# Optimization experiments

Measured on AMD Instinct MI355X. Metric: run time of the kernel, lower is better.

## Reference

```python
import jax, jax.numpy as jnp
import numpy as np

HEADS = 4
DIM_HEAD = 32  # total inner dim; per-head dim = DIM_HEAD // HEADS = 8
SCALE = DIM_HEAD ** -0.5  # faithful to original: scale uses dim_head, not per-head dim


def setup_inputs() -> dict:
    key = jax.random.key(0)
    k_x, k_q, k_kv, k_o, k_pe = jax.random.split(key, 5)
    B, L, dim = 131072, 4, 256
    inner = DIM_HEAD
    x = jax.random.normal(k_x, (B, L, dim), dtype=jnp.float32)
    Wq = jax.random.normal(k_q, (dim, inner), dtype=jnp.float32) * 0.02
    Wkv = jax.random.normal(k_kv, (dim, 2 * inner), dtype=jnp.float32) * 0.02
    Wo = jax.random.normal(k_o, (inner, dim), dtype=jnp.float32) * 0.02
    bo = jnp.zeros((dim,), dtype=jnp.float32)
    pos_emb = jax.random.normal(k_pe, (1, HEADS, L, L), dtype=jnp.float32)
    return {"x": x, "Wq": Wq, "Wkv": Wkv, "Wo": Wo, "bo": bo, "pos_emb": pos_emb}


def reference(x, Wq, Wkv, Wo, bo, pos_emb):
    B, L, dim = x.shape
    dh = DIM_HEAD // HEADS  # per-head dim
    q = x @ Wq                       # [B, L, inner]
    kv = x @ Wkv                     # [B, L, 2*inner]
    k, v = jnp.split(kv, 2, axis=-1)
    # [B, L, inner] -> [B, heads, L, dh]
    split_heads = lambda t: t.reshape(B, L, HEADS, dh).transpose(0, 2, 1, 3)
    q, k, v = map(split_heads, (q, k, v))
    q = q * SCALE
    sim = jnp.einsum('bhid,bhjd->bhij', q, k) + pos_emb  # [B, heads, L, L]
    attn = jax.nn.softmax(sim, axis=-1)
    out = jnp.einsum('bhij,bhjd->bhid', attn, v)         # [B, heads, L, dh]
    out = out.transpose(0, 2, 1, 3).reshape(B, L, HEADS * dh)
    return out @ Wo + bo             # [B, L, dim]
```

## Files before the change

### kernel.cpp

```cpp
#include <hip/hip_runtime.h>
#include <hip/hip_bf16.h>

typedef float  f32x4  __attribute__((ext_vector_type(4)));
typedef __bf16 bf16x8 __attribute__((ext_vector_type(8)));

#define SCALE_QK 0.17677669529663687f


template<int CTRL>
__device__ __forceinline__ float dpp_add(float x) {
  int xi = __builtin_bit_cast(int, x);
  int yi = __builtin_amdgcn_mov_dpp(xi, CTRL, 0xF, 0xF, true);
  return x + __builtin_bit_cast(float, yi);
}

__global__ void pack_weights(const float* __restrict__ Wq, const float* __restrict__ Wkv,
                             const float* __restrict__ Wo, __bf16* __restrict__ wsf) {
  const int item = blockIdx.x * 256 + threadIdx.x;
  const int f = item >> 6, lane = item & 63;
  const int g = lane >> 4, c = lane & 15;
  union { bf16x8 v; __bf16 h[8]; } vv;
  if (f < 48) {
    const int kt = f / 6, ct = f - kt * 6;
    const int n = ct * 16 + c;
    #pragma unroll
    for (int j = 0; j < 8; ++j) {
      const int k = kt * 32 + g * 8 + j;
      vv.h[j] = (__bf16)((n < 32) ? Wq[k * 32 + n] : Wkv[k * 64 + (n - 32)]);
    }
  } else {
    const int ct = f - 48;
    const int n = ct * 16 + c;
    #pragma unroll
    for (int j = 0; j < 8; ++j) vv.h[j] = (__bf16)Wo[(g * 8 + j) * 256 + n];
  }
  *(bf16x8*)&wsf[item * 8] = vv.v;
}

#define FR(f) (*(const bf16x8*)&wfrag[(f) * 512 + lane * 8])
#define MFMA(a, b, cc) __builtin_amdgcn_mfma_f32_16x16x32_bf16((a), (b), (cc), 0, 0, 0)

#define LDS_TOTAL 138496

__global__ __launch_bounds__(256, 1) void fused_stattn(
    const float* __restrict__ x, const __bf16* __restrict__ wsf,
    const float* __restrict__ bo, const float* __restrict__ pe,
    float* __restrict__ out) {
  extern __shared__ char smem[];

  const int tid  = threadIdx.x;
  const int lane = tid & 63;
  const int wv   = tid >> 6;
  const int g    = lane >> 4;
  const int c    = lane & 15;

  __bf16* wfrag = (__bf16*)smem;
  char*   stg   = smem + 65536 + wv * 16640;
  __bf16* aoW   = (__bf16*)(smem + 132096 + wv * 1280);
  float*  bo_l  = (float*)(smem + 137216);
  float*  pe_l  = (float*)(smem + 138240);

  #pragma unroll
  for (int it = 0; it < 16; ++it) {
    const int idx = it * 256 + tid;
    *(bf16x8*)&wfrag[idx * 8] = *(const bf16x8*)&wsf[idx * 8];
  }
  bo_l[tid] = bo[tid];
  if (tid < 64) pe_l[tid] = pe[tid];
  __syncthreads();

  const unsigned stg_lds = (unsigned)(unsigned long long)(void*)stg;

  const int slot  = blockIdx.x * 4 + wv;
  const int tile0 = slot * 32;

  for (int t = 0; t < 32; ++t) {
    const int tile = tile0 + t;

    asm volatile("s_waitcnt lgkmcnt(0)" ::: "memory");
    {
      const float* src = x + (size_t)tile * 4096 + (lane << 2);
      #pragma unroll
      for (int r = 0; r < 16; ++r) {
        __builtin_amdgcn_global_load_lds(
            (const __attribute__((address_space(1))) void*)(src + r * 256),
            (__attribute__((address_space(3))) void*)(unsigned long long)(stg_lds + r * 1040),
            16, 0, 0);
      }
    }
    asm volatile("s_waitcnt vmcnt(0)" ::: "memory");
    __builtin_amdgcn_sched_barrier(0);

    f32x4 acc0 = {0,0,0,0}, acc1 = {0,0,0,0}, acc2 = {0,0,0,0};
    f32x4 acc3 = {0,0,0,0}, acc4 = {0,0,0,0}, acc5 = {0,0,0,0};
    #pragma unroll
    for (int kt = 0; kt < 8; ++kt) {
      const f32x4 va = *(const f32x4*)(stg + c * 1040 + kt * 128 + g * 32);
      const f32x4 vb = *(const f32x4*)(stg + c * 1040 + kt * 128 + g * 32 + 16);
      union { bf16x8 v; __bf16 h[8]; } af;
      #pragma unroll
      for (int j = 0; j < 4; ++j) { af.h[j] = (__bf16)va[j]; af.h[4+j] = (__bf16)vb[j]; }
      acc0 = MFMA(af.v, FR(kt*6+0), acc0);
      acc1 = MFMA(af.v, FR(kt*6+1), acc1);
      acc2 = MFMA(af.v, FR(kt*6+2), acc2);
      acc3 = MFMA(af.v, FR(kt*6+3), acc3);
      acc4 = MFMA(af.v, FR(kt*6+4), acc4);
      acc5 = MFMA(af.v, FR(kt*6+5), acc5);
    }

    const int h0 = c >> 3;
    float ao0[4], ao1[4];
    #pragma unroll
    for (int p = 0; p < 2; ++p) {
      const f32x4 qa = p ? acc1 : acc0;
      const f32x4 ka = p ? acc3 : acc2;
      const f32x4 va = p ? acc5 : acc4;
      const int ph = 2 * p + h0;
      float sim[4][4];
      #pragma unroll
      for (int i = 0; i < 4; ++i)
        #pragma unroll
        for (int j = 0; j < 4; ++j) {
          float pr = qa[i] * ka[j];
          pr = dpp_add<0xB1>(pr);
          pr = dpp_add<0x4E>(pr);
          pr = dpp_add<0x141>(pr);
          sim[i][j] = pr * SCALE_QK + pe_l[ph * 16 + i * 4 + j];
        }
      #pragma unroll
      for (int i = 0; i < 4; ++i) {
        const float m = fmaxf(fmaxf(sim[i][0], sim[i][1]), fmaxf(sim[i][2], sim[i][3]));
        const float e0 = __expf(sim[i][0] - m), e1 = __expf(sim[i][1] - m);
        const float e2 = __expf(sim[i][2] - m), e3 = __expf(sim[i][3] - m);
        const float rs = 1.0f / (e0 + e1 + e2 + e3);
        const float o  = (e0*va[0] + e1*va[1] + e2*va[2] + e3*va[3]) * rs;
        if (p) ao1[i] = o; else ao0[i] = o;
      }
    }

    #pragma unroll
    for (int i = 0; i < 4; ++i) {
      aoW[(g*4 + i) * 40 + c]      = (__bf16)ao0[i];
      aoW[(g*4 + i) * 40 + 16 + c] = (__bf16)ao1[i];
    }
    const bf16x8 a2 = *(const bf16x8*)&aoW[c * 40 + g * 8];

    #pragma unroll
    for (int ct = 0; ct < 16; ++ct) {
      const f32x4 bv = *(const f32x4*)&bo_l[ct * 16 + g * 4];
      f32x4 o = MFMA(FR(48 + ct), a2, bv);
      *(f32x4*)(stg + c * 1040 + ct * 64 + g * 16) = o;
    }

    {
      float* orow = out + (size_t)tile * 4096 + (lane << 2);
      #pragma unroll
      for (int r = 0; r < 16; ++r) {
        const f32x4 v = *(const f32x4*)(stg + r * 1040 + lane * 16);
        *(f32x4*)(orow + r * 256) = v;
      }
    }
  }
}

extern "C" void kernel_launch(void* const* d_in, const int* in_sizes, int n_in,
                              void* d_out, int out_size, void* d_ws, size_t ws_size,
                              hipStream_t stream) {
  const float* x   = (const float*)d_in[0];
  const float* Wq  = (const float*)d_in[1];
  const float* Wkv = (const float*)d_in[2];
  const float* Wo  = (const float*)d_in[3];
  const float* bo  = (const float*)d_in[4];
  const float* pe  = (const float*)d_in[5];
  float* out = (float*)d_out;
  __bf16* wsf = (__bf16*)d_ws;

  (void)hipFuncSetAttribute(reinterpret_cast<const void*>(fused_stattn),
                            hipFuncAttributeMaxDynamicSharedMemorySize, LDS_TOTAL);
  hipLaunchKernelGGL(pack_weights, dim3(16), dim3(256), 0, stream, Wq, Wkv, Wo, wsf);
  hipLaunchKernelGGL(fused_stattn, dim3(256), dim3(256), LDS_TOTAL, stream,
                     x, wsf, bo, pe, out);
}
```

Measured before the change: 230.5 us.

## Double-buffer x tiles with async LDS prefetch and keep Wo fragments in registers

Adds double buffering to the x staging area: while the current tile is computed, the next tile's global_load_lds transfer is already in flight, and a partial vmcnt wait releases only the current buffer. To fit two staging buffers per wave in LDS, the block drops to 3 waves, the Wo fragments move from LDS into registers, and the grid grows to 1024 blocks that walk tiles with a strided loop. Fewer resident waves per CU and higher register pressure are the trade-off for hiding load latency.

```diff
diff --git a/kernel.cpp b/kernel.cpp
--- a/kernel.cpp
+++ b/kernel.cpp
@@ -37,12 +37,12 @@
   *(bf16x8*)&wsf[item * 8] = vv.v;
 }
 
-#define FR(f) (*(const bf16x8*)&wfrag[(f) * 512 + lane * 8])
+#define FR1(f) (*(const bf16x8*)&wfrag1[(f) * 512 + lane * 8])
 #define MFMA(a, b, cc) __builtin_amdgcn_mfma_f32_16x16x32_bf16((a), (b), (cc), 0, 0, 0)
 
-#define LDS_TOTAL 138496
+#define LDS_TOTAL 154112
 
-__global__ __launch_bounds__(256, 1) void fused_stattn(
+__global__ __launch_bounds__(192, 1) void fused_stattn(
     const float* __restrict__ x, const __bf16* __restrict__ wsf,
     const float* __restrict__ bo, const float* __restrict__ pe,
     float* __restrict__ out) {
@@ -54,42 +54,52 @@
   const int g    = lane >> 4;
   const int c    = lane & 15;
 
-  __bf16* wfrag = (__bf16*)smem;
-  char*   stg   = smem + 65536 + wv * 16640;
-  __bf16* aoW   = (__bf16*)(smem + 132096 + wv * 1280);
-  float*  bo_l  = (float*)(smem + 137216);
-  float*  pe_l  = (float*)(smem + 138240);
+  __bf16* wfrag1 = (__bf16*)smem;
+  char*   stg0   = smem + 49152 + wv * 33280;
+  __bf16* aoW    = (__bf16*)(smem + 148992 + wv * 1280);
+  float*  bo_l   = (float*)(smem + 152832);
+  float*  pe_l   = (float*)(smem + 153856);
+
+  bf16x8 wo[16];
+  #pragma unroll
+  for (int i = 0; i < 16; ++i)
+    wo[i] = *(const bf16x8*)&wsf[((48 + i) * 64 + lane) * 8];
 
   #pragma unroll
   for (int it = 0; it < 16; ++it) {
-    const int idx = it * 256 + tid;
-    *(bf16x8*)&wfrag[idx * 8] = *(const bf16x8*)&wsf[idx * 8];
+    const int idx = it * 192 + tid;
+    *(bf16x8*)&wfrag1[idx * 8] = *(const bf16x8*)&wsf[idx * 8];
   }
   bo_l[tid] = bo[tid];
+  if (tid < 64) bo_l[192 + tid] = bo[192 + tid];
   if (tid < 64) pe_l[tid] = pe[tid];
   __syncthreads();
 
-  const unsigned stg_lds = (unsigned)(unsigned long long)(void*)stg;
+  const unsigned stg_lds = (unsigned)(unsigned long long)(void*)stg0;
 
-  const int slot  = blockIdx.x * 4 + wv;
-  const int tile0 = slot * 32;
+  auto stage_tile = [&](unsigned dbase, int tile) {
+    const float* src = x + (size_t)tile * 4096 + (lane << 2);
+    #pragma unroll
+    for (int r = 0; r < 16; ++r) {
+      __builtin_amdgcn_global_load_lds(
+          (const __attribute__((address_space(1))) void*)(src + r * 256),
+          (__attribute__((address_space(3))) void*)(unsigned long long)(dbase + r * 1040),
+          16, 0, 0);
+    }
+  };
 
-  for (int t = 0; t < 32; ++t) {
-    const int tile = tile0 + t;
+  const int slot = blockIdx.x * 3 + wv;
+  int cur = 0;
+  stage_tile(stg_lds, slot);
 
+  for (int tile = slot; tile < 32768; tile += 3072) {
+    const int nt = tile + 3072;
     asm volatile("s_waitcnt lgkmcnt(0)" ::: "memory");
-    {
-      const float* src = x + (size_t)tile * 4096 + (lane << 2);
-      #pragma unroll
-      for (int r = 0; r < 16; ++r) {
-        __builtin_amdgcn_global_load_lds(
-            (const __attribute__((address_space(1))) void*)(src + r * 256),
-            (__attribute__((address_space(3))) void*)(unsigned long long)(stg_lds + r * 1040),
-            16, 0, 0);
-      }
-    }
-    asm volatile("s_waitcnt vmcnt(0)" ::: "memory");
+    if (nt < 32768) stage_tile(stg_lds + (unsigned)((cur ^ 1) * 16640), nt);
+    asm volatile("s_waitcnt vmcnt(16)" ::: "memory");
     __builtin_amdgcn_sched_barrier(0);
+
+    char* stg = stg0 + cur * 16640;
 
     f32x4 acc0 = {0,0,0,0}, acc1 = {0,0,0,0}, acc2 = {0,0,0,0};
     f32x4 acc3 = {0,0,0,0}, acc4 = {0,0,0,0}, acc5 = {0,0,0,0};
@@ -100,12 +110,12 @@
       union { bf16x8 v; __bf16 h[8]; } af;
       #pragma unroll
       for (int j = 0; j < 4; ++j) { af.h[j] = (__bf16)va[j]; af.h[4+j] = (__bf16)vb[j]; }
-      acc0 = MFMA(af.v, FR(kt*6+0), acc0);
-      acc1 = MFMA(af.v, FR(kt*6+1), acc1);
-      acc2 = MFMA(af.v, FR(kt*6+2), acc2);
-      acc3 = MFMA(af.v, FR(kt*6+3), acc3);
-      acc4 = MFMA(af.v, FR(kt*6+4), acc4);
-      acc5 = MFMA(af.v, FR(kt*6+5), acc5);
+      acc0 = MFMA(af.v, FR1(kt*6+0), acc0);
+      acc1 = MFMA(af.v, FR1(kt*6+1), acc1);
+      acc2 = MFMA(af.v, FR1(kt*6+2), acc2);
+      acc3 = MFMA(af.v, FR1(kt*6+3), acc3);
+      acc4 = MFMA(af.v, FR1(kt*6+4), acc4);
+      acc5 = MFMA(af.v, FR1(kt*6+5), acc5);
     }
 
     const int h0 = c >> 3;
@@ -148,7 +158,7 @@
     #pragma unroll
     for (int ct = 0; ct < 16; ++ct) {
       const f32x4 bv = *(const f32x4*)&bo_l[ct * 16 + g * 4];
-      f32x4 o = MFMA(FR(48 + ct), a2, bv);
+      f32x4 o = MFMA(wo[ct], a2, bv);
       *(f32x4*)(stg + c * 1040 + ct * 64 + g * 16) = o;
     }
 
@@ -160,6 +170,8 @@
         *(f32x4*)(orow + r * 256) = v;
       }
     }
+
+    cur ^= 1;
   }
 }
 
@@ -178,6 +190,6 @@
   (void)hipFuncSetAttribute(reinterpret_cast<const void*>(fused_stattn),
                             hipFuncAttributeMaxDynamicSharedMemorySize, LDS_TOTAL);
   hipLaunchKernelGGL(pack_weights, dim3(16), dim3(256), 0, stream, Wq, Wkv, Wo, wsf);
-  hipLaunchKernelGGL(fused_stattn, dim3(256), dim3(256), LDS_TOTAL, stream,
+  hipLaunchKernelGGL(fused_stattn, dim3(1024), dim3(192), LDS_TOTAL, stream,
                      x, wsf, bo, pe, out);
 }
```

Result: faster. 214.2 us (-7.0%).
